# Performance work log

Hardware: AMD Instinct MI355X
Metric: run time of the kernel (lower is better)

## Reference

```python
import jax, jax.numpy as jnp
import numpy as np

EPS = 1.1920929e-07  # torch.finfo(torch.float32).eps
R = 2
K = 2 * R - 1  # 3x3 directional kernels

# kornia normalized sobel kernels (divided by sum of |k| = 8)
_SOBEL_X = np.array([[-1.0, 0.0, 1.0], [-2.0, 0.0, 2.0], [-1.0, 0.0, 1.0]], np.float32) / 8.0
_SOBEL_Y = _SOBEL_X.T.copy()


def _conv2d_same(x, k2d, pad_mode):
    """Depthwise 'same' cross-correlation of x:[B,C,H,W] with a single [kh,kw] kernel."""
    B, C, H, W = x.shape
    kh, kw = k2d.shape
    ph, pw = kh // 2, kw // 2
    xp = jnp.pad(x, ((0, 0), (0, 0), (ph, ph), (pw, pw)), mode=pad_mode)
    xr = xp.reshape(B * C, 1, H + 2 * ph, W + 2 * pw)
    kr = jnp.asarray(k2d, x.dtype)[None, None]  # [1,1,kh,kw]
    y = jax.lax.conv_general_dilated(
        xr, kr, window_strides=(1, 1), padding='VALID',
        dimension_numbers=('NCHW', 'OIHW', 'NCHW'))
    return y.reshape(B, C, H, W)


def _spatial_gradient(x):
    # kornia SpatialGradient(mode='sobel', normalized=True) with replicate padding
    gx = _conv2d_same(x, _SOBEL_X, 'edge')
    gy = _conv2d_same(x, _SOBEL_Y, 'edge')
    return gx, gy


def _edge_theta(true_labels):
    gx, gy = _spatial_gradient(true_labels)
    gxx, _ = _spatial_gradient(gx)       # second_grad_x[:, :, 0]
    gxy, gyy = _spatial_gradient(gy)     # second_grad_y[:, :, 0], [:, :, 1]
    theta = jnp.fmod(
        jnp.arctan(gyy * jnp.sign(-gxy + EPS) / (gxx + EPS)),
        np.float32(np.pi))
    return theta


def _directional_kernels():
    vert = np.zeros((K, K), np.float32); vert[:, R - 1] = 1.0   # ones column
    horiz = np.zeros((K, K), np.float32); horiz[R - 1, :] = 1.0  # ones row
    lead = np.eye(K, dtype=np.float32)
    cnt = np.fliplr(np.eye(K, dtype=np.float32)).copy()
    return horiz, vert, lead, cnt


def setup_inputs() -> dict:
    key = jax.random.key(0)
    k1, k2 = jax.random.split(key)
    true_labels = jax.random.uniform(k1, (8, 2, 1024, 1024), dtype=jnp.float32)
    pred_labels = jax.random.normal(k2, (8, 2, 1024, 1024), dtype=jnp.float32)
    return {"true_labels": true_labels, "pred_labels": pred_labels}


def reference(true_labels, pred_labels):
    theta = _edge_theta(true_labels)
    # quantize edge direction into 5 bins
    thresh_theta = jnp.fmod(jnp.round(theta * (5.0 / np.float32(np.pi))) + 5.0, 5.0)
    exp_preds = jnp.exp(pred_labels)

    horiz_k, vert_k, lead_k, cnt_k = _directional_kernels()
    # kornia filter2D default: reflect padding, no normalization
    horiz_f = _conv2d_same(exp_preds, horiz_k, 'reflect')
    vert_f = _conv2d_same(exp_preds, vert_k, 'reflect')
    lead_f = _conv2d_same(exp_preds, lead_k, 'reflect')
    cnt_f = _conv2d_same(exp_preds, cnt_k, 'reflect')

    horiz_nms = (thresh_theta == 0).astype(exp_preds.dtype) * (exp_preds / (horiz_f + EPS))
    vert_nms = (thresh_theta == 2).astype(exp_preds.dtype) * (exp_preds / (vert_f + EPS))
    lead_nms = (thresh_theta == 3).astype(exp_preds.dtype) * (exp_preds / (lead_f + EPS))
    cnt_nms = (thresh_theta == 1).astype(exp_preds.dtype) * (exp_preds / (cnt_f + EPS))

    # cat along new dim then total sum == sum of the four partial sums
    nms_loss = horiz_nms.sum() + vert_nms.sum() + lead_nms.sum() + cnt_nms.sum()
    return nms_loss
```

## Files before the change

kernel.cpp:

```cpp
#include <hip/hip_runtime.h>

#define HHI 1024
#define WWI 1024
#define NI  16
#define HWSZ (HHI * WWI)
#define EPSF  1.1920929e-07f
#define EPS64 7.62939453125e-06f
#define T1 0.3249196962329063f
#define T2 1.3763819204711735f

#define SW 128
#define RW 16
#define GX  (WWI / SW)
#define GYB (HHI / (RW * 4))
#define NB  (GX * GYB * NI)
#define FR_IMG 8176
#define FR_TOT (FR_IMG * NI)

__device__ __forceinline__ int clampi(int v, int hi) { return v < 0 ? 0 : (v > hi ? hi : v); }
__device__ __forceinline__ int refli(int v, int n)  { return v < 0 ? -v : (v >= n ? 2*n-2-v : v); }
__device__ __forceinline__ float frcp(float x) { return __builtin_amdgcn_rcpf(x); }

#define STAGE(POS, IDX, DOPRED, DOOUT) do {                                           \
    const int i_ = (IDX);                                                             \
    {                                                                                 \
        const int gy_ = clampi(Y0 - 2 + i_, HHI - 1);                                 \
        const float* trow_ = timg + (size_t)gy_ * WWI;                                \
        const float2 cq_ = *(const float2*)(trow_ + x0);                              \
        const float2 lo_ = *(const float2*)(trow_ + cm2);                             \
        const float2 hi_ = *(const float2*)(trow_ + cp2);                             \
        const float w0 = xokl ? lo_.x : cq_.x;                                        \
        const float w1 = xokl ? lo_.y : cq_.x;                                        \
        const float w2 = cq_.x, w3 = cq_.y;                                           \
        const float w4 = xokr ? hi_.x : cq_.y;                                        \
        const float w5 = xokr ? hi_.y : cq_.y;                                        \
        const float s04 = w0 + w4, s13 = w1 + w3;                                     \
        H1[POS][0] = s04 - 2.f * w2;                               \
        H2[POS][0] = s04 + 4.f * s13 + 6.f * w2;                   \
        H3[POS][0] = (w4 - w0) + 2.f * (w3 - w1);                  \
        const float t04 = w1 + w5, t13 = w2 + w4;                                     \
        H1[POS][1] = t04 - 2.f * w3;                                                  \
        H2[POS][1] = t04 + 4.f * t13 + 6.f * w3;                                      \
        H3[POS][1] = (w5 - w1) + 2.f * (w4 - w2);                                     \
    }                                                                                 \
    if (DOPRED) {                                                                     \
        const int gp_ = refli(Y0 + i_ - 3, HHI);                                      \
        const float* prow_ = pimg + (size_t)gp_ * WWI;                                \
        const float2 pc_ = *(const float2*)(prow_ + x0);                              \
        const float2 pl_ = *(const float2*)(prow_ + cm2);                             \
        const float2 ph_ = *(const float2*)(prow_ + cp2);                             \
        E[POS][0] = __expf(xokl ? pl_.y : pc_.y);          \
        E[POS][1] = __expf(pc_.x);                                                    \
        E[POS][2] = __expf(pc_.y);                                                    \
        E[POS][3] = __expf(xokr ? ph_.x : pc_.x);     \
    }                                                                                 \
    if (DOOUT) {                                                                      \
        const int y_ = Y0 + i_ - 4;                                                   \
        const bool my_ = (y_ >= 2) & (y_ <= HHI - 3);                                 \
        const int q0=(POS+1)%5, q1=(POS+2)%5, q2=(POS+3)%5, q3=(POS+4)%5, q4=POS;     \
        const int eT=(POS+3)%5, eM=(POS+4)%5, eB=POS;                                 \
        _Pragma("unroll")                                                             \
        for (int k = 0; k < 2; ++k) {                                                 \
            float gxx = (H1[q0][k]+H1[q4][k]) + 4.f*(H1[q1][k]+H1[q3][k]) + 6.f*H1[q2][k]; \
            float gyy = (H2[q0][k]+H2[q4][k]) - 2.f*H2[q2][k];                        \
            float gxy = (H3[q4][k]-H3[q0][k]) + 2.f*(H3[q3][k]-H3[q1][k]);            \
            float sarg = EPS64 - gxy;                                                 \
            float num = (sarg > 0.f) ? gyy : ((sarg < 0.f) ? -gyy : 0.f);             \
            float v = num * frcp(gxx + EPS64);                                        \
            bool c2v = (v > T2);                                                      \
            bool c1v = (v > T1) & !c2v;                                               \
            bool c0v = (v >= -T1) & (v <= T1);                                        \
            bool c3v = (v < -T2);                                                     \
            bool have = c2v | c1v | c0v | c3v;                       \
            float d1 = c0v ? E[eM][k]   : (c2v ? E[eT][k+1] : (c1v ? E[eT][k+2] : E[eT][k])); \
            float d2 = c0v ? E[eM][k+2] : (c2v ? E[eB][k+1] : (c1v ? E[eB][k]   : E[eB][k+2])); \
            float ec = E[eM][k+1];                                                    \
            float val = ec * frcp(d1 + ec + d2 + EPSF);                               \
            const int x_ = x0 + k;                                                    \
            bool ok = have & my_ & (x_ >= 2) & (x_ <= WWI - 3);                       \
            term += ok ? val : 0.f;                                                   \
        }                                                                             \
    }                                                                                 \
} while (0)

template <bool USE_WS>
__global__ __launch_bounds__(256, 4) void nms_main(
    const float* __restrict__ tru, const float* __restrict__ prd,
    float* __restrict__ partial)
{
    __shared__ float sred[4];
    const int tid  = threadIdx.x;
    const int lane = tid & 63;
    const int wave = tid >> 6;
    const int z = blockIdx.z;
    const float* timg = tru + (size_t)z * HWSZ;
    const float* pimg = prd + (size_t)z * HWSZ;
    float term = 0.f;

    const int x0 = blockIdx.x * SW + lane * 2;
    const int Y0 = blockIdx.y * (RW * 4) + wave * RW;
    const bool xokl = (x0 >= 2);
    const bool xokr = (x0 <= WWI - 4);
    const int cm2 = xokl ? x0 - 2 : 0;
    const int cp2 = xokr ? x0 + 2 : WWI - 2;

    float H1[5][2], H2[5][2], H3[5][2];
    float E[5][4];

    STAGE(0, 0, 0, 0);
    STAGE(1, 1, 0, 0);
    STAGE(2, 2, 1, 0);
    STAGE(3, 3, 1, 0);
    STAGE(4, 4, 1, 1);
    #pragma unroll 1
    for (int g = 1; g < 4; ++g) {
        const int ib = g * 5;
        STAGE(0, ib + 0, 1, 1);
        STAGE(1, ib + 1, 1, 1);
        STAGE(2, ib + 2, 1, 1);
        STAGE(3, ib + 3, 1, 1);
        STAGE(4, ib + 4, 1, 1);
    }

    {
        const int wid = (((z * gridDim.y) + blockIdx.y) * gridDim.x + blockIdx.x) * 4 + wave;
        int fp = wid * 16 + lane;
        const bool valid = (lane < 16) && (fp < FR_TOT);
        if (fp >= FR_TOT) fp = FR_TOT - 1;
        const int fz = fp / FR_IMG;
        const int p  = fp - fz * FR_IMG;
        const float* ftim = tru + (size_t)fz * HWSZ;
        const float* fpim = prd + (size_t)fz * HWSZ;
        int y, x;
        if (p < 2048)      { y = p >> 10;                   x = p & 1023; }
        else if (p < 4096) { y = 1022 + ((p - 2048) >> 10); x = p & 1023; }
        else { int q = p - 4096; y = 2 + (q >> 2); int xi = q & 3; x = (xi < 2) ? xi : 1020 + xi; }

        int R1[3], C1[3], R2[3][3], C2[3][3];
        #pragma unroll
        for (int a = 0; a < 3; ++a) { R1[a] = clampi(y + a - 1, HHI - 1); C1[a] = clampi(x + a - 1, WWI - 1); }
        #pragma unroll
        for (int a = 0; a < 3; ++a)
            #pragma unroll
            for (int e = 0; e < 3; ++e) {
                R2[a][e] = clampi(R1[a] + e - 1, HHI - 1);
                C2[a][e] = clampi(C1[a] + e - 1, WWI - 1);
            }
        const int hx[3] = {-1, 0, 1}, vx[3] = {1, 2, 1};
        const int hy[3] = {1, 2, 1},  vy[3] = {-1, 0, 1};
        float gxu[3][3], gyu[3][3];
        #pragma unroll
        for (int a = 0; a < 3; ++a)
            #pragma unroll
            for (int b = 0; b < 3; ++b) {
                float sx = 0.f, sy = 0.f;
                #pragma unroll
                for (int e = 0; e < 3; ++e)
                    #pragma unroll
                    for (int f = 0; f < 3; ++f) {
                        const int wx = hx[f] * vx[e], wy = hy[f] * vy[e];
                        if (wx | wy) {
                            float tv = ftim[(size_t)R2[a][e] * WWI + C2[b][f]];
                            if (wx) sx += (float)wx * tv;
                            if (wy) sy += (float)wy * tv;
                        }
                    }
                gxu[a][b] = sx; gyu[a][b] = sy;
            }
        float gxx = 0.f, gxy = 0.f, gyy = 0.f;
        #pragma unroll
        for (int a = 0; a < 3; ++a)
            #pragma unroll
            for (int b = 0; b < 3; ++b) {
                const int w1 = hx[b] * vx[a], w2 = hy[b] * vy[a];
                if (w1) { gxx += (float)w1 * gxu[a][b]; gxy += (float)w1 * gyu[a][b]; }
                if (w2) { gyy += (float)w2 * gyu[a][b]; }
            }
        float sarg = EPS64 - gxy;
        float num = (sarg > 0.f) ? gyy : ((sarg < 0.f) ? -gyy : 0.f);
        float v = num * frcp(gxx + EPS64);
        bool c2v = (v > T2);
        bool c1v = (v > T1) & !c2v;
        bool c0v = (v >= -T1) & (v <= T1);
        bool c3v = (v < -T2);
        bool have = c2v | c1v | c0v | c3v;
        int r1 = c0v ? y : refli(y - 1, HHI);
        int r2 = c0v ? y : refli(y + 1, HHI);
        int xm = refli(x - 1, WWI), xp = refli(x + 1, WWI);
        int co1 = c2v ? x : (c1v ? xp : xm);
        int co2 = c2v ? x : (c1v ? xm : xp);
        float ecf = __expf(fpim[(size_t)y * WWI + x]);
        float d1f = __expf(fpim[(size_t)r1 * WWI + co1]);
        float d2f = __expf(fpim[(size_t)r2 * WWI + co2]);
        float fval = ecf * frcp(d1f + ecf + d2f + EPSF);
        term += (have & valid) ? fval : 0.f;
    }

    for (int off = 32; off; off >>= 1) term += __shfl_down(term, off, 64);
    if (lane == 0) sred[wave] = term;
    __syncthreads();
    if (tid == 0) {
        float b = sred[0] + sred[1] + sred[2] + sred[3];
        if (USE_WS) {
            partial[((size_t)z * gridDim.y + blockIdx.y) * gridDim.x + blockIdx.x] = b;
        } else {
            atomicAdd(partial, b);
        }
    }
}

__global__ __launch_bounds__(1024) void reduce_kernel(
    const float* __restrict__ partial, float* __restrict__ out)
{
    __shared__ float s_red[16];
    float s = 0.f;
    for (int i = threadIdx.x; i < NB; i += 1024) s += partial[i];
    for (int off = 32; off; off >>= 1) s += __shfl_down(s, off, 64);
    if ((threadIdx.x & 63) == 0) s_red[threadIdx.x >> 6] = s;
    __syncthreads();
    if (threadIdx.x == 0) {
        float b = 0.f;
        #pragma unroll
        for (int i = 0; i < 16; ++i) b += s_red[i];
        out[0] = b;
    }
}

extern "C" void kernel_launch(void* const* d_in, const int* in_sizes, int n_in,
                              void* d_out, int out_size, void* d_ws, size_t ws_size,
                              hipStream_t stream) {
    const float* tru = (const float*)d_in[0];
    const float* prd = (const float*)d_in[1];
    float* out = (float*)d_out;
    dim3 grid(GX, GYB, NI);
    dim3 block(256, 1, 1);
    if (ws_size >= (size_t)NB * sizeof(float)) {
        float* ws = (float*)d_ws;
        hipLaunchKernelGGL(nms_main<true>, grid, block, 0, stream, tru, prd, ws);
        hipLaunchKernelGGL(reduce_kernel, dim3(1), dim3(1024), 0, stream, ws, out);
    } else {
        hipMemsetAsync(out, 0, sizeof(float), stream);
        hipLaunchKernelGGL(nms_main<false>, grid, block, 0, stream, tru, prd, out);
    }
}
```

Baseline: 79.78 us.

## Stage exp(pred) tile in shared memory as fp16 and gather neighbours from LDS

Replaces per-thread register rolling of exp(pred) values with a cooperative prologue that loads a 66x132 halo tile of pred, applies exp, and stores it in shared memory as half precision. Each output then gathers only its center and two selected neighbours from LDS, using direction-dependent indices. Launch bounds are raised to 8 blocks per CU. This removes redundant global loads and exp work in the main loop, at the cost of a sync, a serialized prologue, and fp16 rounding of exp values, which can overflow to inf for large inputs and changes precision.

```diff
diff --git a/kernel.cpp b/kernel.cpp
--- a/kernel.cpp
+++ b/kernel.cpp
@@ -1,4 +1,5 @@
 #include <hip/hip_runtime.h>
+#include <hip/hip_fp16.h>
 
 #define HHI 1024
 #define WWI 1024
@@ -9,19 +10,18 @@
 #define T1 0.3249196962329063f
 #define T2 1.3763819204711735f
 
-#define SW 128
-#define RW 16
-#define GX  (WWI / SW)
-#define GYB (HHI / (RW * 4))
-#define NB  (GX * GYB * NI)
+#define GX2  8
+#define GYB2 16
+#define NB   (GX2 * GYB2 * NI)
 #define FR_IMG 8176
 #define FR_TOT (FR_IMG * NI)
+#define LROW 132
 
 __device__ __forceinline__ int clampi(int v, int hi) { return v < 0 ? 0 : (v > hi ? hi : v); }
 __device__ __forceinline__ int refli(int v, int n)  { return v < 0 ? -v : (v >= n ? 2*n-2-v : v); }
 __device__ __forceinline__ float frcp(float x) { return __builtin_amdgcn_rcpf(x); }
 
-#define STAGE(POS, IDX, DOPRED, DOOUT) do {                                           \
+#define STAGE(POS, IDX, DOOUT) do {                                                   \
     const int i_ = (IDX);                                                             \
     {                                                                                 \
         const int gy_ = clampi(Y0 - 2 + i_, HHI - 1);                                 \
@@ -43,22 +43,11 @@
         H2[POS][1] = t04 + 4.f * t13 + 6.f * w3;                                      \
         H3[POS][1] = (w5 - w1) + 2.f * (w4 - w2);                                     \
     }                                                                                 \
-    if (DOPRED) {                                                                     \
-        const int gp_ = refli(Y0 + i_ - 3, HHI);                                      \
-        const float* prow_ = pimg + (size_t)gp_ * WWI;                                \
-        const float2 pc_ = *(const float2*)(prow_ + x0);                              \
-        const float2 pl_ = *(const float2*)(prow_ + cm2);                             \
-        const float2 ph_ = *(const float2*)(prow_ + cp2);                             \
-        E[POS][0] = __expf(xokl ? pl_.y : pc_.y);          \
-        E[POS][1] = __expf(pc_.x);                                                    \
-        E[POS][2] = __expf(pc_.y);                                                    \
-        E[POS][3] = __expf(xokr ? ph_.x : pc_.x);     \
-    }                                                                                 \
     if (DOOUT) {                                                                      \
         const int y_ = Y0 + i_ - 4;                                                   \
         const bool my_ = (y_ >= 2) & (y_ <= HHI - 3);                                 \
+        const int ly = wave * 16 + i_ - 3;                 \
         const int q0=(POS+1)%5, q1=(POS+2)%5, q2=(POS+3)%5, q3=(POS+4)%5, q4=POS;     \
-        const int eT=(POS+3)%5, eM=(POS+4)%5, eB=POS;                                 \
         _Pragma("unroll")                                                             \
         for (int k = 0; k < 2; ++k) {                                                 \
             float gxx = (H1[q0][k]+H1[q4][k]) + 4.f*(H1[q1][k]+H1[q3][k]) + 6.f*H1[q2][k]; \
@@ -72,9 +61,15 @@
             bool c0v = (v >= -T1) & (v <= T1);                                        \
             bool c3v = (v < -T2);                                                     \
             bool have = c2v | c1v | c0v | c3v;                       \
-            float d1 = c0v ? E[eM][k]   : (c2v ? E[eT][k+1] : (c1v ? E[eT][k+2] : E[eT][k])); \
-            float d2 = c0v ? E[eM][k+2] : (c2v ? E[eB][k+1] : (c1v ? E[eB][k]   : E[eB][k+2])); \
-            float ec = E[eM][k+1];                                                    \
+                          \
+            const int lx = 2 * lane + k + 2;                                          \
+            const int dr1 = c0v ? 0 : -1;                                             \
+            const int dc1 = c0v ? -1 : (c2v ? 0 : (c1v ? 1 : -1));                    \
+            const int i1 = (ly + dr1) * LROW + lx + dc1;                              \
+            const int i2 = (ly + (c0v ? 0 : 1)) * LROW + lx - dc1;                    \
+            float d1 = __half2float(sE[i1]);                                          \
+            float d2 = __half2float(sE[i2]);                                          \
+            float ec = __half2float(sE[ly * LROW + lx]);                              \
             float val = ec * frcp(d1 + ec + d2 + EPSF);                               \
             const int x_ = x0 + k;                                                    \
             bool ok = have & my_ & (x_ >= 2) & (x_ <= WWI - 3);                       \
@@ -84,46 +79,70 @@
 } while (0)
 
 template <bool USE_WS>
-__global__ __launch_bounds__(256, 4) void nms_main(
+__global__ __launch_bounds__(256, 8) void nms_main(
     const float* __restrict__ tru, const float* __restrict__ prd,
     float* __restrict__ partial)
 {
+    __shared__ __align__(8) __half sE[66 * LROW];
     __shared__ float sred[4];
     const int tid  = threadIdx.x;
     const int lane = tid & 63;
     const int wave = tid >> 6;
-    const int z = blockIdx.z;
+    const int z  = blockIdx.z;
+    const int bx = blockIdx.x, by = blockIdx.y;
     const float* timg = tru + (size_t)z * HWSZ;
     const float* pimg = prd + (size_t)z * HWSZ;
+    const int X0  = bx * 128;
+    const int Y0b = by * 64;
     float term = 0.f;
 
-    const int x0 = blockIdx.x * SW + lane * 2;
-    const int Y0 = blockIdx.y * (RW * 4) + wave * RW;
+    {
+        const bool xedge = (bx == 0) | (bx == GX2 - 1);
+        for (int pidx = tid; pidx < 66 * 66; pidx += 256) {
+            const int r  = pidx / 66;
+            const int cp = pidx - r * 66;
+            const int gr = refli(Y0b - 1 + r, HHI);
+            const float* prow = pimg + (size_t)gr * WWI;
+            float e0, e1;
+            if (xedge) {
+                e0 = prow[refli(X0 - 2 + 2 * cp, WWI)];
+                e1 = prow[refli(X0 - 1 + 2 * cp, WWI)];
+            } else {
+                const float2 pv = *(const float2*)(prow + (X0 - 2 + 2 * cp));
+                e0 = pv.x; e1 = pv.y;
+            }
+            __half2 h2 = __floats2half2_rn(__expf(e0), __expf(e1));
+            *reinterpret_cast<__half2*>(&sE[r * LROW + 2 * cp]) = h2;
+        }
+    }
+    __syncthreads();
+
+    const int x0 = X0 + lane * 2;
+    const int Y0 = Y0b + wave * 16;
     const bool xokl = (x0 >= 2);
     const bool xokr = (x0 <= WWI - 4);
     const int cm2 = xokl ? x0 - 2 : 0;
     const int cp2 = xokr ? x0 + 2 : WWI - 2;
 
     float H1[5][2], H2[5][2], H3[5][2];
-    float E[5][4];
-
-    STAGE(0, 0, 0, 0);
-    STAGE(1, 1, 0, 0);
-    STAGE(2, 2, 1, 0);
-    STAGE(3, 3, 1, 0);
-    STAGE(4, 4, 1, 1);
+
+    STAGE(0, 0, 0);
+    STAGE(1, 1, 0);
+    STAGE(2, 2, 0);
+    STAGE(3, 3, 0);
+    STAGE(4, 4, 1);
     #pragma unroll 1
     for (int g = 1; g < 4; ++g) {
         const int ib = g * 5;
-        STAGE(0, ib + 0, 1, 1);
-        STAGE(1, ib + 1, 1, 1);
-        STAGE(2, ib + 2, 1, 1);
-        STAGE(3, ib + 3, 1, 1);
-        STAGE(4, ib + 4, 1, 1);
+        STAGE(0, ib + 0, 1);
+        STAGE(1, ib + 1, 1);
+        STAGE(2, ib + 2, 1);
+        STAGE(3, ib + 3, 1);
+        STAGE(4, ib + 4, 1);
     }
 
     {
-        const int wid = (((z * gridDim.y) + blockIdx.y) * gridDim.x + blockIdx.x) * 4 + wave;
+        const int wid = (((z * gridDim.y) + by) * gridDim.x + bx) * 4 + wave;
         int fp = wid * 16 + lane;
         const bool valid = (lane < 16) && (fp < FR_TOT);
         if (fp >= FR_TOT) fp = FR_TOT - 1;
@@ -202,7 +221,7 @@
     if (tid == 0) {
         float b = sred[0] + sred[1] + sred[2] + sred[3];
         if (USE_WS) {
-            partial[((size_t)z * gridDim.y + blockIdx.y) * gridDim.x + blockIdx.x] = b;
+            partial[((size_t)z * gridDim.y + by) * gridDim.x + bx] = b;
         } else {
             atomicAdd(partial, b);
         }
@@ -232,7 +251,7 @@
     const float* tru = (const float*)d_in[0];
     const float* prd = (const float*)d_in[1];
     float* out = (float*)d_out;
-    dim3 grid(GX, GYB, NI);
+    dim3 grid(GX2, GYB2, NI);
     dim3 block(256, 1, 1);
     if (ws_size >= (size_t)NB * sizeof(float)) {
         float* ws = (float*)d_ws;
```

Result: slower. 131.8 us (+65.2%).
